# Optimization experiments

Hardware: AMD Instinct MI355X
Metric: run time of the kernel (lower is better)

## Reference

```python
import jax, jax.numpy as jnp
import numpy as np

N = 100000   # nodes
E = 400000   # edges per relation
K = 2        # n_hop relations
D = 256      # in_dim
ATT = 64     # att_dim
L = 3        # n_layer
H1, H2 = 128, 64
EPS = 1e-5
NEG_SLOPE = 0.01


def setup_inputs() -> dict:
    key = jax.random.key(0)
    ks = jax.random.split(key, 16)
    s = 1.0 / np.sqrt(D)
    return {
        "x": jax.random.normal(ks[0], (N, D), jnp.float32),
        "edges_index": jax.random.randint(ks[1], (K, 2, E), 0, N),
        "edges_weight": jax.random.uniform(ks[2], (K, E), jnp.float32),
        "bn_gamma": jnp.ones((D,), jnp.float32),
        "bn_beta": jnp.zeros((D,), jnp.float32),
        "gcn_W": jax.random.normal(ks[3], (L, D, D), jnp.float32) * s,
        "gcn_b": jnp.zeros((L, D), jnp.float32),
        "att_lin_W": jax.random.normal(ks[4], (L, K, D, ATT), jnp.float32) * s,
        "att_lin_b": jnp.zeros((L, K, ATT), jnp.float32),
        "att_q": jax.random.normal(ks[5], (L, K, ATT), jnp.float32) * (1.0 / np.sqrt(ATT)),
        "proj_W1": jax.random.normal(ks[6], (D, H1), jnp.float32) * s,
        "proj_b1": jnp.zeros((H1,), jnp.float32),
        "proj_W2": jax.random.normal(ks[7], (H1, H2), jnp.float32) * (1.0 / np.sqrt(H1)),
        "proj_b2": jnp.zeros((H2,), jnp.float32),
    }


def _gcn_aggregate(row, col, w, xw):
    # symmetric gcn_norm on adj_t (add_self_loops=False):
    # deg[i] = sum of w over edges with col == i
    deg = jax.ops.segment_sum(w, col, num_segments=N)
    dinv = jnp.where(deg > 0, 1.0 / jnp.sqrt(deg), 0.0)
    norm = dinv[col] * w * dinv[row]                       # [E]
    # out[c] += norm * xw[r]
    return jax.ops.segment_sum(norm[:, None] * xw[row], col, num_segments=N)


def reference(x, edges_index, edges_weight, bn_gamma, bn_beta, gcn_W, gcn_b,
              att_lin_W, att_lin_b, att_q, proj_W1, proj_b1, proj_W2, proj_b2):
    # BatchNorm1d (training-mode batch stats)
    mu = jnp.mean(x, axis=0)
    var = jnp.mean((x - mu) ** 2, axis=0)
    h = (x - mu) / jnp.sqrt(var + EPS) * bn_gamma + bn_beta   # [N, D]

    rows = edges_index[:, 0, :]  # [K, E]
    cols = edges_index[:, 1, :]

    for i in range(L):
        xw = h @ gcn_W[i]                                     # shared transform [N, D]
        # per-relation sparse aggregation, vmapped over K
        xs = jax.vmap(_gcn_aggregate, in_axes=(0, 0, 0, None))(
            rows, cols, edges_weight, xw) + gcn_b[i]          # [K, N, D]
        # HanAtt: softmax over hops of per-node scores
        keys = jnp.tanh(jnp.einsum('knd,kdh->knh', xs, att_lin_W[i]) + att_lin_b[i][:, None, :])
        sim = jnp.einsum('knh,kh->kn', keys, att_q[i])        # [K, N]
        alpha = jax.nn.softmax(sim, axis=0)                   # softmax over K
        h = jnp.einsum('knd,kn->nd', xs, alpha)               # [N, D]
        h = jax.nn.relu(h)

    h = jax.nn.leaky_relu(h @ proj_W1 + proj_b1, NEG_SLOPE)
    h = jax.nn.leaky_relu(h @ proj_W2 + proj_b2, NEG_SLOPE)
    return h
```

## Files before the change

### kernel.cpp

```cpp
#include <hip/hip_runtime.h>
#include <hip/hip_bf16.h>
#include <math.h>

#define NN 100000
#define EE 400000
#define KD 2
#define DD 256
#define ATTD 64
#define LL 3
#define HH1 128
#define HH2 64
#define EPSV 1e-5f
#define SLOPE 0.01f
#define KN (KD * NN)
#define WFP 33554432.0f

typedef short short8 __attribute__((ext_vector_type(8)));
typedef float floatx4 __attribute__((ext_vector_type(4)));
typedef unsigned int u32x4 __attribute__((ext_vector_type(4)));
typedef unsigned short u16;
typedef unsigned int u32;
typedef unsigned long long u64;

__device__ __forceinline__ u16 f2bf(float f) {
    u32 u = __float_as_uint(f);
    return (u16)((u + 0x7fffu + ((u >> 16) & 1u)) >> 16);
}
__device__ __forceinline__ float bf2f(u16 h) {
    return __uint_as_float((u32)h << 16);
}

__global__ void bn_stats(const float* __restrict__ x, float* __restrict__ sums) {
    int d = threadIdx.x;
    int r0 = blockIdx.x * 125;
    float s = 0.f, sq = 0.f;
    for (int r = r0; r < r0 + 125; ++r) {
        float v = x[(size_t)r * DD + d];
        s += v; sq += v * v;
    }
    atomicAdd(&sums[d], s);
    atomicAdd(&sums[DD + d], sq);
}

__global__ void bn_apply(const float* __restrict__ x, const float* __restrict__ sums,
                         const float* __restrict__ gamma, const float* __restrict__ beta,
                         u16* __restrict__ h_hi, u16* __restrict__ h_lo) {
    size_t i = (size_t)blockIdx.x * blockDim.x + threadIdx.x;
    const float inv_n = 1.f / NN;
    int dq = (int)(i & 63) * 4;
    float4 xv = ((const float4*)x)[i];
    ushort4 hv, lv;
    float* xp = (float*)&xv;
    u16* hp = (u16*)&hv; u16* lp = (u16*)&lv;
#pragma unroll
    for (int j = 0; j < 4; ++j) {
        int d = dq + j;
        float mu = sums[d] * inv_n;
        float var = sums[DD + d] * inv_n - mu * mu;
        float inv = rsqrtf(var + EPSV);
        float v = (xp[j] - mu) * inv * gamma[d] + beta[d];
        u16 hb = f2bf(v);
        hp[j] = hb;
        lp[j] = f2bf(v - bf2f(hb));
    }
    ((ushort4*)h_hi)[i] = hv;
    ((ushort4*)h_lo)[i] = lv;
}

__global__ void deg_count(const int* __restrict__ ei, const float* __restrict__ w,
                          u64* __restrict__ dc) {
    int i = blockIdx.x * blockDim.x + threadIdx.x;
    if (i >= KD * EE) return;
    int k = i / EE, e = i - k * EE;
    int col = ei[(size_t)k * 2 * EE + EE + e];
    u64 wfp = (u64)__float2uint_rn(w[i] * WFP);
    atomicAdd(&dc[k * NN + col], ((u64)1 << 32) | wfp);
}

__global__ void dinv_pack(const u64* __restrict__ dc, float* __restrict__ dinv,
                          int* __restrict__ starts) {
    int i = blockIdx.x * blockDim.x + threadIdx.x;
    if (i >= KN) return;
    u64 p = dc[i];
    float deg = (float)(u32)p * (1.f / WFP);
    dinv[i] = deg > 0.f ? 1.f / sqrtf(deg) : 0.f;
    starts[i] = (int)(p >> 32);
}

#define SCAN_NB ((KN + 255) / 256)
__global__ void scan_blocks(int* __restrict__ starts, int* __restrict__ bsums) {
    __shared__ int tmp[256];
    int t = threadIdx.x;
    int idx = blockIdx.x * 256 + t;
    int v = (idx < KN) ? starts[idx] : 0;
    tmp[t] = v;
    __syncthreads();
#pragma unroll
    for (int off = 1; off < 256; off <<= 1) {
        int s = (t >= off) ? tmp[t - off] : 0;
        __syncthreads();
        tmp[t] += s;
        __syncthreads();
    }
    if (idx < KN) starts[idx] = tmp[t] - v;
    if (t == 255) bsums[blockIdx.x] = tmp[255];
}

__global__ void scan_sums(int* __restrict__ bsums) {
    __shared__ int tmp[1024];
    int t = threadIdx.x;
    int v = (t < SCAN_NB) ? bsums[t] : 0;
    tmp[t] = v;
    __syncthreads();
#pragma unroll
    for (int off = 1; off < 1024; off <<= 1) {
        int s = (t >= off) ? tmp[t - off] : 0;
        __syncthreads();
        tmp[t] += s;
        __syncthreads();
    }
    if (t < SCAN_NB) bsums[t] = tmp[t] - v;
}

__global__ void scan_add(int* __restrict__ starts, const int* __restrict__ bsums) {
    int idx = blockIdx.x * 256 + threadIdx.x;
    if (idx < KN) starts[idx] += bsums[blockIdx.x];
}

__global__ void csr_fill(const int* __restrict__ ei, const float* __restrict__ w,
                         const float* __restrict__ dinv,
                         int* __restrict__ starts, int2* __restrict__ edata) {
    int i = blockIdx.x * blockDim.x + threadIdx.x;
    if (i >= KD * EE) return;
    int k = i / EE, e = i - k * EE;
    const int* eik = ei + (size_t)k * 2 * EE;
    int row = eik[e], col = eik[EE + e];
    float nv = dinv[k * NN + col] * w[i] * dinv[k * NN + row];
    int pos = atomicAdd(&starts[k * NN + col], 1);
    edata[pos] = make_int2(row, __float_as_int(nv));
}

__device__ __forceinline__ void fma_row8(float4& a0, float4& a1, uint4 w, float nv) {
    float2 f0 = __bfloat1622float2(*(const __hip_bfloat162*)&w.x);
    float2 f1 = __bfloat1622float2(*(const __hip_bfloat162*)&w.y);
    float2 f2 = __bfloat1622float2(*(const __hip_bfloat162*)&w.z);
    float2 f3 = __bfloat1622float2(*(const __hip_bfloat162*)&w.w);
    a0.x += nv * f0.x; a0.y += nv * f0.y; a0.z += nv * f1.x; a0.w += nv * f1.y;
    a1.x += nv * f2.x; a1.y += nv * f2.y; a1.z += nv * f3.x; a1.w += nv * f3.y;
}

__global__ __launch_bounds__(256) void gather_agg(
        const int* __restrict__ starts, const int2* __restrict__ edata,
        const u16* __restrict__ xw, u16* __restrict__ xs) {
    int wv = blockIdx.x * 4 + (threadIdx.x >> 6);
    int lane = threadIdx.x & 63;
    int half = lane >> 5, l32 = lane & 31;
    int widx = wv * 2 + half;
    if (widx >= KN) return;
    int begin = widx ? starts[widx - 1] : 0;
    int end = starts[widx];
    int deg = end - begin;
    float4 acc0 = make_float4(0.f, 0.f, 0.f, 0.f);
    float4 acc1 = make_float4(0.f, 0.f, 0.f, 0.f);

    int2 ed = (l32 < deg) ? edata[begin + l32] : make_int2(0, 0);
    int dmain = deg > 32 ? 32 : deg;
    int base = half << 5;

    int j = 0;
    for (; j + 4 <= dmain; j += 4) {
        int r0 = __shfl(ed.x, base + j),     r1 = __shfl(ed.x, base + j + 1);
        int r2 = __shfl(ed.x, base + j + 2), r3 = __shfl(ed.x, base + j + 3);
        float n0 = __int_as_float(__shfl(ed.y, base + j));
        float n1 = __int_as_float(__shfl(ed.y, base + j + 1));
        float n2 = __int_as_float(__shfl(ed.y, base + j + 2));
        float n3 = __int_as_float(__shfl(ed.y, base + j + 3));
        uint4 w0 = *(const uint4*)(xw + (size_t)r0 * DD + l32 * 8);
        uint4 w1 = *(const uint4*)(xw + (size_t)r1 * DD + l32 * 8);
        uint4 w2 = *(const uint4*)(xw + (size_t)r2 * DD + l32 * 8);
        uint4 w3 = *(const uint4*)(xw + (size_t)r3 * DD + l32 * 8);
        fma_row8(acc0, acc1, w0, n0);
        fma_row8(acc0, acc1, w1, n1);
        fma_row8(acc0, acc1, w2, n2);
        fma_row8(acc0, acc1, w3, n3);
    }
    for (; j < dmain; ++j) {
        int r = __shfl(ed.x, base + j);
        float nv = __int_as_float(__shfl(ed.y, base + j));
        uint4 w = *(const uint4*)(xw + (size_t)r * DD + l32 * 8);
        fma_row8(acc0, acc1, w, nv);
    }
    for (int e = begin + 32; e < end; ++e) {
        int2 ee = edata[e];
        float nv = __int_as_float(ee.y);
        uint4 w = *(const uint4*)(xw + (size_t)ee.x * DD + l32 * 8);
        fma_row8(acc0, acc1, w, nv);
    }

    u32x4 st;
    st.x = (u32)f2bf(acc0.x) | ((u32)f2bf(acc0.y) << 16);
    st.y = (u32)f2bf(acc0.z) | ((u32)f2bf(acc0.w) << 16);
    st.z = (u32)f2bf(acc1.x) | ((u32)f2bf(acc1.y) << 16);
    st.w = (u32)f2bf(acc1.z) | ((u32)f2bf(acc1.w) << 16);
    *(u32x4*)(xs + (size_t)widx * DD + l32 * 8) = st;
}

#define GCN_T (LL * DD * DD)
#define ATT_T (LL * KD * DD * ATTD)
#define P1_T  (DD * HH1)
#define P2_T  (HH1 * HH2)
#define WC_TOTAL (GCN_T + ATT_T + P1_T + P2_T)
__device__ __forceinline__ void wconv1(const float* __restrict__ W, u16* __restrict__ Wt,
                                       int i, int Kd, int Nc) {
    int kk = i / Nc, n = i - kk * Nc;
    Wt[(size_t)n * Kd + kk] = f2bf(W[i]);
}
__global__ void wconv_all(const float* __restrict__ gcnW, u16* __restrict__ gcnWb,
                          const float* __restrict__ attW, u16* __restrict__ attWb,
                          const float* __restrict__ pW1, u16* __restrict__ pW1b,
                          const float* __restrict__ pW2, u16* __restrict__ pW2b) {
    int gid = blockIdx.x * 256 + threadIdx.x;
    if (gid >= WC_TOTAL) return;
    if (gid < GCN_T) {
        int l = gid >> 16, i = gid & 65535;
        wconv1(gcnW + (size_t)l * DD * DD, gcnWb + (size_t)l * DD * DD, i, DD, DD);
    } else if (gid < GCN_T + ATT_T) {
        int g = gid - GCN_T;
        int lk = g >> 14, i = g & 16383;
        wconv1(attW + (size_t)lk * DD * ATTD, attWb + (size_t)lk * ATTD * DD, i, DD, ATTD);
    } else if (gid < GCN_T + ATT_T + P1_T) {
        wconv1(pW1, pW1b, gid - (GCN_T + ATT_T), DD, HH1);
    } else {
        wconv1(pW2, pW2b, gid - (GCN_T + ATT_T + P1_T), HH1, HH2);
    }
}

__global__ void att_bias_fold(const float* __restrict__ attW, const float* __restrict__ attb,
                              const float* __restrict__ gcnb, float* __restrict__ batt) {
    int lk = blockIdx.x;
    int a = threadIdx.x;
    int l = lk >> 1;
    const float* W = attW + (size_t)lk * DD * ATTD;
    const float* gb = gcnb + l * DD;
    float s = attb[lk * ATTD + a];
    for (int d = 0; d < DD; ++d) s += gb[d] * W[d * ATTD + a];
    batt[lk * ATTD + a] = s;
}

#define LDSP 40

template<int BN_, int MODE, bool PRESPLIT, bool BIAS, int ACT>
__global__ __launch_bounds__(256) void gemm_mfma(
        const float* __restrict__ A,
        const u16* __restrict__ Ahi, const u16* __restrict__ Alo,
        const u16* __restrict__ Bt, const float* __restrict__ bias,
        float* __restrict__ Cf, u16* __restrict__ Cb,
        int M, int Kd, int Nc) {
    constexpr int JW = BN_ / 64;
    __shared__ u16 AsHi[64 * LDSP];
    __shared__ u16 AsLo[64 * LDSP];
    __shared__ u16 Bs[BN_ * LDSP];

    const int tid = threadIdx.x;
    const int lane = tid & 63, wx = tid >> 6;
    const int lane15 = lane & 15, quad = lane >> 4;
    const int bm = blockIdx.x * 64;
    const int bn = blockIdx.y * BN_;

    floatx4 acc[4][JW];
#pragma unroll
    for (int i = 0; i < 4; ++i)
#pragma unroll
        for (int j = 0; j < JW; ++j) acc[i][j] = (floatx4){0.f, 0.f, 0.f, 0.f};

    for (int k0 = 0; k0 < Kd; k0 += 32) {
        if constexpr (PRESPLIT) {
            {
                int m = tid >> 2, ko = (tid & 3) << 3;
                uint4 vh = make_uint4(0, 0, 0, 0), vl = make_uint4(0, 0, 0, 0);
                if (bm + m < M) {
                    vh = *(const uint4*)(Ahi + (size_t)(bm + m) * Kd + k0 + ko);
                    vl = *(const uint4*)(Alo + (size_t)(bm + m) * Kd + k0 + ko);
                }
                *(uint4*)(void*)(AsHi + m * LDSP + ko) = vh;
                *(uint4*)(void*)(AsLo + m * LDSP + ko) = vl;
            }
        } else {
#pragma unroll
            for (int t = tid; t < 512; t += 256) {
                int m = t >> 3, k4 = (t & 7) << 2;
                float4 v = make_float4(0.f, 0.f, 0.f, 0.f);
                if (bm + m < M) v = *(const float4*)(A + (size_t)(bm + m) * Kd + k0 + k4);
                u16 h0 = f2bf(v.x), h1 = f2bf(v.y), h2 = f2bf(v.z), h3 = f2bf(v.w);
                *(ushort4*)(void*)(AsHi + m * LDSP + k4) = make_ushort4(h0, h1, h2, h3);
                u16 l0 = f2bf(v.x - bf2f(h0)), l1 = f2bf(v.y - bf2f(h1));
                u16 l2 = f2bf(v.z - bf2f(h2)), l3 = f2bf(v.w - bf2f(h3));
                *(ushort4*)(void*)(AsLo + m * LDSP + k4) = make_ushort4(l0, l1, l2, l3);
            }
        }
#pragma unroll
        for (int t = tid; t < BN_ * 4; t += 256) {
            int n = t >> 2, ko = (t & 3) << 3;
            uint4 w = *(const uint4*)(Bt + (size_t)(bn + n) * Kd + k0 + ko);
            *(uint4*)(void*)(Bs + n * LDSP + ko) = w;
        }
        __syncthreads();

        const u16* pA  = AsHi + lane15 * LDSP + quad * 8;
        const u16* pAl = AsLo + lane15 * LDSP + quad * 8;
        const u16* pB  = Bs + (wx * (BN_ / 4) + lane15) * LDSP + quad * 8;
        short8 b[JW];
#pragma unroll
        for (int j = 0; j < JW; ++j) b[j] = *(const short8*)(pB + j * 16 * LDSP);
#pragma unroll
        for (int i = 0; i < 4; ++i) {
            short8 a = *(const short8*)(pA + i * 16 * LDSP);
#pragma unroll
            for (int j = 0; j < JW; ++j)
                acc[i][j] = __builtin_amdgcn_mfma_f32_16x16x32_bf16(a, b[j], acc[i][j], 0, 0, 0);
        }
#pragma unroll
        for (int i = 0; i < 4; ++i) {
            short8 a = *(const short8*)(pAl + i * 16 * LDSP);
#pragma unroll
            for (int j = 0; j < JW; ++j)
                acc[i][j] = __builtin_amdgcn_mfma_f32_16x16x32_bf16(a, b[j], acc[i][j], 0, 0, 0);
        }
        __syncthreads();
    }

#pragma unroll
    for (int i = 0; i < 4; ++i) {
#pragma unroll
        for (int r = 0; r < 4; ++r) {
            int row = bm + i * 16 + quad * 4 + r;
            if (row >= M) continue;
#pragma unroll
            for (int j = 0; j < JW; ++j) {
                int col = bn + wx * (BN_ / 4) + j * 16 + lane15;
                float v = acc[i][j][r];
                if constexpr (BIAS) v += bias[col];
                if constexpr (ACT == 1) v = v > 0.f ? v : SLOPE * v;
                if constexpr (MODE == 0) Cf[(size_t)row * Nc + col] = v;
                else                     Cb[(size_t)row * Nc + col] = f2bf(v);
            }
        }
    }
}

__global__ __launch_bounds__(256) void att_combine(
        const u16* __restrict__ xs, const u16* __restrict__ Bt,
        const float* __restrict__ batt, const float* __restrict__ qv,
        const float* __restrict__ gcnb,
        u16* __restrict__ h_hi, u16* __restrict__ h_lo) {
    __shared__ u16 As[2 * 64 * LDSP];
    __shared__ u16 Bs[2 * 64 * LDSP];
    __shared__ float simbuf[KD][2][64];

    const int tid = threadIdx.x;
    const int lane = tid & 63, waveid = tid >> 6;
    const int kw = waveid >> 1, ch = waveid & 1;
    const int lane15 = lane & 15, quad = lane >> 4;
    const int bm = blockIdx.x * 64;

    floatx4 acc[4][2];
#pragma unroll
    for (int i = 0; i < 4; ++i)
#pragma unroll
        for (int j = 0; j < 2; ++j) acc[i][j] = (floatx4){0.f, 0.f, 0.f, 0.f};

    for (int k0 = 0; k0 < DD; k0 += 32) {
#pragma unroll
        for (int it = 0; it < 2; ++it) {
            int t = tid + it * 256;
            int k = t >> 8, m = (t >> 2) & 63, ko = (t & 3) << 3;
            uint4 v = make_uint4(0, 0, 0, 0);
            if (bm + m < NN)
                v = *(const uint4*)(xs + ((size_t)k * NN + bm + m) * DD + k0 + ko);
            *(uint4*)(void*)(As + (k * 64 + m) * LDSP + ko) = v;
        }
#pragma unroll
        for (int it = 0; it < 2; ++it) {
            int t = tid + it * 256;
            int k = t >> 8, c = (t >> 2) & 63, ko = (t & 3) << 3;
            uint4 v = *(const uint4*)(Bt + ((size_t)k * ATTD + c) * DD + k0 + ko);
            *(uint4*)(void*)(Bs + (k * 64 + c) * LDSP + ko) = v;
        }
        __syncthreads();

        const u16* pA = As + (kw * 64 + lane15) * LDSP + quad * 8;
        const u16* pB = Bs + (kw * 64 + ch * 32 + lane15) * LDSP + quad * 8;
        short8 b0 = *(const short8*)(pB);
        short8 b1 = *(const short8*)(pB + 16 * LDSP);
#pragma unroll
        for (int i = 0; i < 4; ++i) {
            short8 a = *(const short8*)(pA + i * 16 * LDSP);
            acc[i][0] = __builtin_amdgcn_mfma_f32_16x16x32_bf16(a, b0, acc[i][0], 0, 0, 0);
            acc[i][1] = __builtin_amdgcn_mfma_f32_16x16x32_bf16(a, b1, acc[i][1], 0, 0, 0);
        }
        __syncthreads();
    }

#pragma unroll
    for (int i = 0; i < 4; ++i) {
#pragma unroll
        for (int r = 0; r < 4; ++r) {
            float p = 0.f;
#pragma unroll
            for (int j = 0; j < 2; ++j) {
                int col = ch * 32 + j * 16 + lane15;
                float v = acc[i][j][r] + batt[kw * ATTD + col];
                float ex = __expf(2.f * v);
                float th = 1.f - 2.f / (ex + 1.f);
                p += th * qv[kw * ATTD + col];
            }
            p += __shfl_xor(p, 1, 64);
            p += __shfl_xor(p, 2, 64);
            p += __shfl_xor(p, 4, 64);
            p += __shfl_xor(p, 8, 64);
            if (lane15 == 0) simbuf[kw][ch][i * 16 + quad * 4 + r] = p;
        }
    }
    __syncthreads();

#pragma unroll 4
    for (int it = 0; it < 8; ++it) {
        int item = tid + it * 256;
        int row = item >> 5, c8 = item & 31;
        int grow = bm + row;
        if (grow >= NN) continue;
        float s0 = simbuf[0][0][row] + simbuf[0][1][row];
        float s1 = simbuf[1][0][row] + simbuf[1][1][row];
        float m = fmaxf(s0, s1);
        float e0 = __expf(s0 - m), e1 = __expf(s1 - m);
        float inv = 1.f / (e0 + e1);
        float a0 = e0 * inv, a1 = e1 * inv;
        uint4 x0 = *(const uint4*)(xs + (size_t)grow * DD + c8 * 8);
        uint4 x1 = *(const uint4*)(xs + ((size_t)NN + grow) * DD + c8 * 8);
        const float* bp = gcnb + c8 * 8;
        uint4 hiw, low;
        u16* hp = (u16*)&hiw; u16* lp = (u16*)&low;
        const u32* xp0 = (const u32*)&x0; const u32* xp1 = (const u32*)&x1;
#pragma unroll
        for (int j = 0; j < 4; ++j) {
            float2 f0 = __bfloat1622float2(*(const __hip_bfloat162*)&xp0[j]);
            float2 f1 = __bfloat1622float2(*(const __hip_bfloat162*)&xp1[j]);
            float ra = fmaxf(0.f, a0 * f0.x + a1 * f1.x + bp[2 * j]);
            float rb = fmaxf(0.f, a0 * f0.y + a1 * f1.y + bp[2 * j + 1]);
            u16 ha = f2bf(ra), hb = f2bf(rb);
            hp[2 * j] = ha; hp[2 * j + 1] = hb;
            lp[2 * j] = f2bf(ra - bf2f(ha));
            lp[2 * j + 1] = f2bf(rb - bf2f(hb));
        }
        *(uint4*)(h_hi + (size_t)grow * DD + c8 * 8) = hiw;
        *(uint4*)(h_lo + (size_t)grow * DD + c8 * 8) = low;
    }
}

extern "C" void kernel_launch(void* const* d_in, const int* in_sizes, int n_in,
                              void* d_out, int out_size, void* d_ws, size_t ws_size,
                              hipStream_t stream) {
    const float* x     = (const float*)d_in[0];
    const int*   ei    = (const int*)d_in[1];
    const float* ew    = (const float*)d_in[2];
    const float* gamma = (const float*)d_in[3];
    const float* beta  = (const float*)d_in[4];
    const float* gcn_W = (const float*)d_in[5];
    const float* gcn_b = (const float*)d_in[6];
    const float* att_W = (const float*)d_in[7];
    const float* att_b = (const float*)d_in[8];
    const float* att_q = (const float*)d_in[9];
    const float* pW1   = (const float*)d_in[10];
    const float* pb1   = (const float*)d_in[11];
    const float* pW2   = (const float*)d_in[12];
    const float* pb2   = (const float*)d_in[13];
    float* out = (float*)d_out;

    char* wsb = (char*)d_ws;
    size_t off = 0;
    auto alloc = [&](size_t bytes) -> void* {
        void* p = wsb + off;
        off += (bytes + 255) & ~(size_t)255;
        return p;
    };
    u16*   xs    = (u16*)alloc((size_t)KD * NN * DD * 2);
    u16*   h_hi  = (u16*)alloc((size_t)NN * DD * 2);
    u16*   h_lo  = (u16*)alloc((size_t)NN * DD * 2);
    u16*   xw    = (u16*)alloc((size_t)NN * DD * 2);
    float* p1tmp = (float*)xw;
    float* dinv  = (float*)alloc((size_t)KN * 4);
    int*   starts= (int*)alloc(((size_t)KN + 1) * 4);
    u64*   dc    = (u64*)alloc((size_t)KN * 8);
    int2*  edata = (int2*)alloc((size_t)KD * EE * 8);
    float* bnsums= (float*)alloc(2 * DD * 4);
    u16*   gcnWb = (u16*)alloc((size_t)LL * DD * DD * 2);
    u16*   attWb = (u16*)alloc((size_t)LL * KD * ATTD * DD * 2);
    u16*   pW1b  = (u16*)alloc((size_t)HH1 * DD * 2);
    u16*   pW2b  = (u16*)alloc((size_t)HH2 * HH1 * 2);
    float* batt  = (float*)alloc((size_t)LL * KD * ATTD * 4);
    int*   bsums = (int*)alloc((size_t)SCAN_NB * 4);

    wconv_all<<<(WC_TOTAL + 255) / 256, 256, 0, stream>>>(
        gcn_W, gcnWb, att_W, attWb, pW1, pW1b, pW2, pW2b);
    att_bias_fold<<<LL * KD, ATTD, 0, stream>>>(att_W, att_b, gcn_b, batt);

    hipMemsetAsync(bnsums, 0, 2 * DD * 4, stream);
    bn_stats<<<800, 256, 0, stream>>>(x, bnsums);
    bn_apply<<<25000, 256, 0, stream>>>(x, bnsums, gamma, beta, h_hi, h_lo);

    hipMemsetAsync(dc, 0, (size_t)KN * 8, stream);
    deg_count<<<(KD * EE + 255) / 256, 256, 0, stream>>>(ei, ew, dc);
    dinv_pack<<<(KN + 255) / 256, 256, 0, stream>>>(dc, dinv, starts);
    scan_blocks<<<SCAN_NB, 256, 0, stream>>>(starts, bsums);
    scan_sums<<<1, 1024, 0, stream>>>(bsums);
    scan_add<<<SCAN_NB, 256, 0, stream>>>(starts, bsums);
    csr_fill<<<(KD * EE + 255) / 256, 256, 0, stream>>>(ei, ew, dinv, starts, edata);

    const int MB64 = (NN + 63) / 64;
    for (int l = 0; l < LL; ++l) {
        gemm_mfma<256, 1, true, false, 0><<<dim3(MB64, 1), 256, 0, stream>>>(
            nullptr, h_hi, h_lo, gcnWb + (size_t)l * DD * DD, nullptr,
            nullptr, xw, NN, DD, DD);
        gather_agg<<<(KN + 7) / 8, 256, 0, stream>>>(starts, edata, xw, xs);
        att_combine<<<MB64, 256, 0, stream>>>(
            xs, attWb + (size_t)l * KD * ATTD * DD,
            batt + (size_t)l * KD * ATTD, att_q + (size_t)l * KD * ATTD,
            gcn_b + l * DD, h_hi, h_lo);
    }

    gemm_mfma<128, 0, true, true, 1><<<dim3(MB64, 1), 256, 0, stream>>>(
        nullptr, h_hi, h_lo, pW1b, pb1, p1tmp, nullptr, NN, DD, HH1);
    gemm_mfma<64, 0, false, true, 1><<<dim3(MB64, 1), 256, 0, stream>>>(
        p1tmp, nullptr, nullptr, pW2b, pb2, out, nullptr, NN, HH1, HH2);
}
```

Baseline: 929.9 us.

## Fuse sparse gather aggregation into attention-combine kernel via shared memory

Merges the per-relation CSR gather aggregation into the attention/combine kernel. Each block now aggregates 32 nodes for both relations straight into LDS, then runs the MFMA attention projection and softmax combine from LDS. This drops the xs intermediate buffer and its global write and read of 2*N*D bf16 per layer, plus one launch per layer. In exchange each block holds more LDS, tiles are smaller (32 rows), and each half-wave handles 8 nodes serially, which may lower latency hiding for the irregular gathers.

```diff
diff --git a/kernel.cpp b/kernel.cpp
--- a/kernel.cpp
+++ b/kernel.cpp
@@ -30,6 +30,15 @@
     return __uint_as_float((u32)h << 16);
 }
 
+__device__ __forceinline__ void fma_row8_(float4& a0, float4& a1, uint4 w, float nv) {
+    float2 f0 = __bfloat1622float2(*(const __hip_bfloat162*)&w.x);
+    float2 f1 = __bfloat1622float2(*(const __hip_bfloat162*)&w.y);
+    float2 f2 = __bfloat1622float2(*(const __hip_bfloat162*)&w.z);
+    float2 f3 = __bfloat1622float2(*(const __hip_bfloat162*)&w.w);
+    a0.x += nv * f0.x; a0.y += nv * f0.y; a0.z += nv * f1.x; a0.w += nv * f1.y;
+    a1.x += nv * f2.x; a1.y += nv * f2.y; a1.z += nv * f3.x; a1.w += nv * f3.y;
+}
+
 __global__ void bn_stats(const float* __restrict__ x, float* __restrict__ sums) {
     int d = threadIdx.x;
     int r0 = blockIdx.x * 125;
@@ -138,71 +147,6 @@
     float nv = dinv[k * NN + col] * w[i] * dinv[k * NN + row];
     int pos = atomicAdd(&starts[k * NN + col], 1);
     edata[pos] = make_int2(row, __float_as_int(nv));
-}
-
-__device__ __forceinline__ void fma_row8(float4& a0, float4& a1, uint4 w, float nv) {
-    float2 f0 = __bfloat1622float2(*(const __hip_bfloat162*)&w.x);
-    float2 f1 = __bfloat1622float2(*(const __hip_bfloat162*)&w.y);
-    float2 f2 = __bfloat1622float2(*(const __hip_bfloat162*)&w.z);
-    float2 f3 = __bfloat1622float2(*(const __hip_bfloat162*)&w.w);
-    a0.x += nv * f0.x; a0.y += nv * f0.y; a0.z += nv * f1.x; a0.w += nv * f1.y;
-    a1.x += nv * f2.x; a1.y += nv * f2.y; a1.z += nv * f3.x; a1.w += nv * f3.y;
-}
-
-__global__ __launch_bounds__(256) void gather_agg(
-        const int* __restrict__ starts, const int2* __restrict__ edata,
-        const u16* __restrict__ xw, u16* __restrict__ xs) {
-    int wv = blockIdx.x * 4 + (threadIdx.x >> 6);
-    int lane = threadIdx.x & 63;
-    int half = lane >> 5, l32 = lane & 31;
-    int widx = wv * 2 + half;
-    if (widx >= KN) return;
-    int begin = widx ? starts[widx - 1] : 0;
-    int end = starts[widx];
-    int deg = end - begin;
-    float4 acc0 = make_float4(0.f, 0.f, 0.f, 0.f);
-    float4 acc1 = make_float4(0.f, 0.f, 0.f, 0.f);
-
-    int2 ed = (l32 < deg) ? edata[begin + l32] : make_int2(0, 0);
-    int dmain = deg > 32 ? 32 : deg;
-    int base = half << 5;
-
-    int j = 0;
-    for (; j + 4 <= dmain; j += 4) {
-        int r0 = __shfl(ed.x, base + j),     r1 = __shfl(ed.x, base + j + 1);
-        int r2 = __shfl(ed.x, base + j + 2), r3 = __shfl(ed.x, base + j + 3);
-        float n0 = __int_as_float(__shfl(ed.y, base + j));
-        float n1 = __int_as_float(__shfl(ed.y, base + j + 1));
-        float n2 = __int_as_float(__shfl(ed.y, base + j + 2));
-        float n3 = __int_as_float(__shfl(ed.y, base + j + 3));
-        uint4 w0 = *(const uint4*)(xw + (size_t)r0 * DD + l32 * 8);
-        uint4 w1 = *(const uint4*)(xw + (size_t)r1 * DD + l32 * 8);
-        uint4 w2 = *(const uint4*)(xw + (size_t)r2 * DD + l32 * 8);
-        uint4 w3 = *(const uint4*)(xw + (size_t)r3 * DD + l32 * 8);
-        fma_row8(acc0, acc1, w0, n0);
-        fma_row8(acc0, acc1, w1, n1);
-        fma_row8(acc0, acc1, w2, n2);
-        fma_row8(acc0, acc1, w3, n3);
-    }
-    for (; j < dmain; ++j) {
-        int r = __shfl(ed.x, base + j);
-        float nv = __int_as_float(__shfl(ed.y, base + j));
-        uint4 w = *(const uint4*)(xw + (size_t)r * DD + l32 * 8);
-        fma_row8(acc0, acc1, w, nv);
-    }
-    for (int e = begin + 32; e < end; ++e) {
-        int2 ee = edata[e];
-        float nv = __int_as_float(ee.y);
-        uint4 w = *(const uint4*)(xw + (size_t)ee.x * DD + l32 * 8);
-        fma_row8(acc0, acc1, w, nv);
-    }
-
-    u32x4 st;
-    st.x = (u32)f2bf(acc0.x) | ((u32)f2bf(acc0.y) << 16);
-    st.y = (u32)f2bf(acc0.z) | ((u32)f2bf(acc0.w) << 16);
-    st.z = (u32)f2bf(acc1.x) | ((u32)f2bf(acc1.y) << 16);
-    st.w = (u32)f2bf(acc1.z) | ((u32)f2bf(acc1.w) << 16);
-    *(u32x4*)(xs + (size_t)widx * DD + l32 * 8) = st;
 }
 
 #define GCN_T (LL * DD * DD)
@@ -348,37 +292,96 @@
     }
 }
 
-__global__ __launch_bounds__(256) void att_combine(
-        const u16* __restrict__ xs, const u16* __restrict__ Bt,
+#define BMF 32
+#define ALDS 264
+
+__global__ __launch_bounds__(256) void att_fused(
+        const int* __restrict__ starts, const int2* __restrict__ edata,
+        const u16* __restrict__ xw, const u16* __restrict__ Bt,
         const float* __restrict__ batt, const float* __restrict__ qv,
         const float* __restrict__ gcnb,
         u16* __restrict__ h_hi, u16* __restrict__ h_lo) {
-    __shared__ u16 As[2 * 64 * LDSP];
+    __shared__ u16 As[KD * BMF * ALDS];
     __shared__ u16 Bs[2 * 64 * LDSP];
-    __shared__ float simbuf[KD][2][64];
+    __shared__ float simbuf[KD][2][BMF];
 
     const int tid = threadIdx.x;
     const int lane = tid & 63, waveid = tid >> 6;
+    const int l32 = tid & 31;
+    const int hid = tid >> 5;
+    const int base = lane & 32;
+    const int bm = blockIdx.x * BMF;
+
+    {
+        const int kk = hid >> 2;
+        const int r0 = (hid & 3) * 8;
+        const int widx0 = kk * NN + bm + r0;
+        int sv = 0;
+        if (l32 < 9) {
+            int idx = widx0 - 1 + l32;
+            sv = idx >= 0 ? starts[idx] : 0;
+        }
+        int2 ed[8];
+#pragma unroll
+        for (int g = 0; g < 8; ++g) {
+            int b = __shfl(sv, base + g), e = __shfl(sv, base + g + 1);
+            ed[g] = (l32 < e - b) ? edata[b + l32] : make_int2(0, 0);
+        }
+#pragma unroll
+        for (int g = 0; g < 8; ++g) {
+            int b = __shfl(sv, base + g), e = __shfl(sv, base + g + 1);
+            int deg = e - b;
+            int dmain = deg > 32 ? 32 : deg;
+            float4 a0 = make_float4(0.f, 0.f, 0.f, 0.f);
+            float4 a1 = make_float4(0.f, 0.f, 0.f, 0.f);
+            int j = 0;
+            for (; j + 4 <= dmain; j += 4) {
+                int s0 = __shfl(ed[g].x, base + j),     s1 = __shfl(ed[g].x, base + j + 1);
+                int s2 = __shfl(ed[g].x, base + j + 2), s3 = __shfl(ed[g].x, base + j + 3);
+                float n0 = __int_as_float(__shfl(ed[g].y, base + j));
+                float n1 = __int_as_float(__shfl(ed[g].y, base + j + 1));
+                float n2 = __int_as_float(__shfl(ed[g].y, base + j + 2));
+                float n3 = __int_as_float(__shfl(ed[g].y, base + j + 3));
+                uint4 w0 = *(const uint4*)(xw + (size_t)s0 * DD + l32 * 8);
+                uint4 w1 = *(const uint4*)(xw + (size_t)s1 * DD + l32 * 8);
+                uint4 w2 = *(const uint4*)(xw + (size_t)s2 * DD + l32 * 8);
+                uint4 w3 = *(const uint4*)(xw + (size_t)s3 * DD + l32 * 8);
+                fma_row8_(a0, a1, w0, n0);
+                fma_row8_(a0, a1, w1, n1);
+                fma_row8_(a0, a1, w2, n2);
+                fma_row8_(a0, a1, w3, n3);
+            }
+            for (; j < dmain; ++j) {
+                int s0 = __shfl(ed[g].x, base + j);
+                float nv = __int_as_float(__shfl(ed[g].y, base + j));
+                uint4 w = *(const uint4*)(xw + (size_t)s0 * DD + l32 * 8);
+                fma_row8_(a0, a1, w, nv);
+            }
+            for (int e2 = b + 32; e2 < e; ++e2) {
+                int2 ee = edata[e2];
+                float nv = __int_as_float(ee.y);
+                uint4 w = *(const uint4*)(xw + (size_t)ee.x * DD + l32 * 8);
+                fma_row8_(a0, a1, w, nv);
+            }
+            u32x4 st;
+            st.x = (u32)f2bf(a0.x) | ((u32)f2bf(a0.y) << 16);
+            st.y = (u32)f2bf(a0.z) | ((u32)f2bf(a0.w) << 16);
+            st.z = (u32)f2bf(a1.x) | ((u32)f2bf(a1.y) << 16);
+            st.w = (u32)f2bf(a1.z) | ((u32)f2bf(a1.w) << 16);
+            *(u32x4*)(void*)(As + (kk * BMF + r0 + g) * ALDS + l32 * 8) = st;
+        }
+    }
+    __syncthreads();
+
     const int kw = waveid >> 1, ch = waveid & 1;
     const int lane15 = lane & 15, quad = lane >> 4;
-    const int bm = blockIdx.x * 64;
-
-    floatx4 acc[4][2];
-#pragma unroll
-    for (int i = 0; i < 4; ++i)
+    floatx4 acc[2][2];
+#pragma unroll
+    for (int i = 0; i < 2; ++i)
 #pragma unroll
         for (int j = 0; j < 2; ++j) acc[i][j] = (floatx4){0.f, 0.f, 0.f, 0.f};
 
     for (int k0 = 0; k0 < DD; k0 += 32) {
-#pragma unroll
-        for (int it = 0; it < 2; ++it) {
-            int t = tid + it * 256;
-            int k = t >> 8, m = (t >> 2) & 63, ko = (t & 3) << 3;
-            uint4 v = make_uint4(0, 0, 0, 0);
-            if (bm + m < NN)
-                v = *(const uint4*)(xs + ((size_t)k * NN + bm + m) * DD + k0 + ko);
-            *(uint4*)(void*)(As + (k * 64 + m) * LDSP + ko) = v;
-        }
 #pragma unroll
         for (int it = 0; it < 2; ++it) {
             int t = tid + it * 256;
@@ -387,14 +390,13 @@
             *(uint4*)(void*)(Bs + (k * 64 + c) * LDSP + ko) = v;
         }
         __syncthreads();
-
-        const u16* pA = As + (kw * 64 + lane15) * LDSP + quad * 8;
+        const u16* pA = As + (kw * BMF + lane15) * ALDS + k0 + quad * 8;
         const u16* pB = Bs + (kw * 64 + ch * 32 + lane15) * LDSP + quad * 8;
         short8 b0 = *(const short8*)(pB);
         short8 b1 = *(const short8*)(pB + 16 * LDSP);
 #pragma unroll
-        for (int i = 0; i < 4; ++i) {
-            short8 a = *(const short8*)(pA + i * 16 * LDSP);
+        for (int i = 0; i < 2; ++i) {
+            short8 a = *(const short8*)(pA + i * 16 * ALDS);
             acc[i][0] = __builtin_amdgcn_mfma_f32_16x16x32_bf16(a, b0, acc[i][0], 0, 0, 0);
             acc[i][1] = __builtin_amdgcn_mfma_f32_16x16x32_bf16(a, b1, acc[i][1], 0, 0, 0);
         }
@@ -402,7 +404,7 @@
     }
 
 #pragma unroll
-    for (int i = 0; i < 4; ++i) {
+    for (int i = 0; i < 2; ++i) {
 #pragma unroll
         for (int r = 0; r < 4; ++r) {
             float p = 0.f;
@@ -423,20 +425,19 @@
     }
     __syncthreads();
 
-#pragma unroll 4
-    for (int it = 0; it < 8; ++it) {
+#pragma unroll
+    for (int it = 0; it < 4; ++it) {
         int item = tid + it * 256;
         int row = item >> 5, c8 = item & 31;
         int grow = bm + row;
-        if (grow >= NN) continue;
         float s0 = simbuf[0][0][row] + simbuf[0][1][row];
         float s1 = simbuf[1][0][row] + simbuf[1][1][row];
         float m = fmaxf(s0, s1);
         float e0 = __expf(s0 - m), e1 = __expf(s1 - m);
         float inv = 1.f / (e0 + e1);
         float a0 = e0 * inv, a1 = e1 * inv;
-        uint4 x0 = *(const uint4*)(xs + (size_t)grow * DD + c8 * 8);
-        uint4 x1 = *(const uint4*)(xs + ((size_t)NN + grow) * DD + c8 * 8);
+        uint4 x0 = *(const uint4*)(As + row * ALDS + c8 * 8);
+        uint4 x1 = *(const uint4*)(As + (BMF + row) * ALDS + c8 * 8);
         const float* bp = gcnb + c8 * 8;
         uint4 hiw, low;
         u16* hp = (u16*)&hiw; u16* lp = (u16*)&low;
@@ -483,7 +484,6 @@
         off += (bytes + 255) & ~(size_t)255;
         return p;
     };
-    u16*   xs    = (u16*)alloc((size_t)KD * NN * DD * 2);
     u16*   h_hi  = (u16*)alloc((size_t)NN * DD * 2);
     u16*   h_lo  = (u16*)alloc((size_t)NN * DD * 2);
     u16*   xw    = (u16*)alloc((size_t)NN * DD * 2);
@@ -517,13 +517,13 @@
     csr_fill<<<(KD * EE + 255) / 256, 256, 0, stream>>>(ei, ew, dinv, starts, edata);
 
     const int MB64 = (NN + 63) / 64;
+    const int MBF  = NN / BMF;
     for (int l = 0; l < LL; ++l) {
         gemm_mfma<256, 1, true, false, 0><<<dim3(MB64, 1), 256, 0, stream>>>(
             nullptr, h_hi, h_lo, gcnWb + (size_t)l * DD * DD, nullptr,
             nullptr, xw, NN, DD, DD);
-        gather_agg<<<(KN + 7) / 8, 256, 0, stream>>>(starts, edata, xw, xs);
-        att_combine<<<MB64, 256, 0, stream>>>(
-            xs, attWb + (size_t)l * KD * ATTD * DD,
+        att_fused<<<MBF, 256, 0, stream>>>(
+            starts, edata, xw, attWb + (size_t)l * KD * ATTD * DD,
             batt + (size_t)l * KD * ATTD, att_q + (size_t)l * KD * ATTD,
             gcn_b + l * DD, h_hi, h_lo);
     }
```

After: 911.8 us. Within noise of the previous version (-1.9%).
